# Optimization experiments

Hardware: AMD Instinct MI355X
Metric: run time of the kernel (lower is better)

## Reference

```python
import jax, jax.numpy as jnp
import numpy as np

E_DIM = 640   # RNA-FM embedding dim
H = 256       # hidden_dim
L = 3         # num_gcn_layers
LN_EPS = 1e-5


def _layer_norm(x, g, b):
    mu = jnp.mean(x, axis=-1, keepdims=True)
    var = jnp.mean((x - mu) ** 2, axis=-1, keepdims=True)
    return (x - mu) * jax.lax.rsqrt(var + LN_EPS) * g + b


def setup_inputs() -> dict:
    key = jax.random.key(0)
    ks = jax.random.split(key, 20)
    B, S = 4, 256

    def w(k, shape):
        fan_in = shape[-2] if len(shape) >= 2 else shape[-1]
        return jax.random.normal(k, shape, dtype=jnp.float32) / np.sqrt(fan_in)

    inp = {
        "embeddings": jax.random.normal(ks[0], (B, S, E_DIM), dtype=jnp.float32),
        "bp_priors": jax.random.uniform(ks[1], (B, S, S), dtype=jnp.float32),
        "sequence_lengths": jnp.full((B,), S, dtype=jnp.int32),
        # FeatureEncoder: Linear(640, 512) -> ReLU -> Linear(512, 256)
        "enc_w1": w(ks[2], (E_DIM, 2 * H)), "enc_b1": jnp.zeros((2 * H,), jnp.float32),
        "enc_w2": w(ks[3], (2 * H, H)),     "enc_b2": jnp.zeros((H,), jnp.float32),
        # GCN layers (stacked over L)
        "gcn_wself": w(ks[4], (L, H, H)), "gcn_bself": jnp.zeros((L, H), jnp.float32),
        "gcn_wedge": w(ks[5], (L, H, H)), "gcn_bedge": jnp.zeros((L, H), jnp.float32),
        "gcn_ln_g": jnp.ones((L, H), jnp.float32), "gcn_ln_b": jnp.zeros((L, H), jnp.float32),
        # PairwiseScorer MLP: Linear(2H+1, H) -> ReLU -> Linear(H, H//2) -> ReLU -> Linear(H//2, 1)
        "mlp_w1": w(ks[6], (2 * H + 1, H)), "mlp_b1": jnp.zeros((H,), jnp.float32),
        "mlp_w2": w(ks[7], (H, H // 2)),    "mlp_b2": jnp.zeros((H // 2,), jnp.float32),
        "mlp_w3": w(ks[8], (H // 2, 1)),    "mlp_b3": jnp.zeros((1,), jnp.float32),
    }
    return inp


def reference(embeddings, bp_priors, sequence_lengths,
              enc_w1, enc_b1, enc_w2, enc_b2,
              gcn_wself, gcn_bself, gcn_wedge, gcn_bedge, gcn_ln_g, gcn_ln_b,
              mlp_w1, mlp_b1, mlp_w2, mlp_b2, mlp_w3, mlp_b3):
    # FeatureEncoder
    h = jax.nn.relu(embeddings @ enc_w1 + enc_b1) @ enc_w2 + enc_b2  # [B,S,H]

    # GCN layers: self GEMM + adjacency (bp_priors) aggregated neighbor GEMM
    for l in range(L):
        self_f = h @ gcn_wself[l] + gcn_bself[l]
        neigh_f = jnp.einsum('bij,bjh->bih', bp_priors, h @ gcn_wedge[l] + gcn_bedge[l])
        h = _layer_norm(jax.nn.relu(self_f + neigh_f), gcn_ln_g[l], gcn_ln_b[l])

    # PairwiseScorer: concat([node_i, node_j, prior]) @ W1 split into three partial products
    # (mathematically identical to the expand-concat-MLP in the torch module).
    hi = h @ mlp_w1[:H]           # [B,S,H] contribution of node_i
    hj = h @ mlp_w1[H:2 * H]      # [B,S,H] contribution of node_j
    p = jax.nn.relu(hi[:, :, None, :] + hj[:, None, :, :]
                    + bp_priors[..., None] * mlp_w1[2 * H] + mlp_b1)  # [B,S,S,H]
    p = jax.nn.relu(p @ mlp_w2 + mlp_b2)                              # [B,S,S,H//2]
    bp_scores = (p @ mlp_w3 + mlp_b3)[..., 0]                         # [B,S,S]
    return bp_scores
```

## Files before the change

### kernel.cpp

```cpp
#include <hip/hip_runtime.h>

typedef __attribute__((ext_vector_type(8))) short short8;
typedef __attribute__((ext_vector_type(4))) float f32x4;

__device__ __forceinline__ unsigned short f2bf(float x) {
    union { float f; unsigned u; } v; v.f = x;
    unsigned r = v.u + 0x7FFF + ((v.u >> 16) & 1);
    return (unsigned short)(r >> 16);
}
__device__ __forceinline__ float bf2f(unsigned short h) {
    union { unsigned u; float f; } v; v.u = ((unsigned)h) << 16;
    return v.f;
}

template<bool RELU>
__global__ __launch_bounds__(256)
void gemm32(const float* __restrict__ A, const float* __restrict__ B0,
            const float* __restrict__ bias0, float* __restrict__ C0,
            const float* __restrict__ B1, const float* __restrict__ bias1,
            float* __restrict__ C1,
            int M, int N, int K, int aB, int bB, int cB, int nxHalf)
{
    int bx = blockIdx.x;
    const float* B = B0; const float* bias = bias0; float* C = C0;
    if (nxHalf && bx >= nxHalf) { bx -= nxHalf; B = B1; bias = bias1; C = C1; }
    A += (long)blockIdx.z * aB;
    B += (long)blockIdx.z * bB;
    C += (long)blockIdx.z * cB;
    const int m0 = blockIdx.y * 32, n0 = bx * 64;

    __shared__ __align__(16) float As[32][36];
    __shared__ __align__(16) float Bs[32][68];
    const int tid = threadIdx.x;
    const int tx = tid & 15, ty = tid >> 4;
    float acc[2][4] = {};

    for (int k0 = 0; k0 < K; k0 += 32) {
        {
            int row = tid >> 3, kq = (tid & 7) << 2;
            float4 v = *(const float4*)&A[(long)(m0 + row) * K + k0 + kq];
            As[kq + 0][row] = v.x; As[kq + 1][row] = v.y;
            As[kq + 2][row] = v.z; As[kq + 3][row] = v.w;
        }
#pragma unroll
        for (int q = 0; q < 2; ++q) {
            int f = tid * 2 + q;
            int kk = f >> 4, nn = (f & 15) << 2;
            *(float4*)&Bs[kk][nn] = *(const float4*)&B[(long)(k0 + kk) * N + n0 + nn];
        }
        __syncthreads();
#pragma unroll
        for (int k = 0; k < 32; ++k) {
            float2 a2 = *(const float2*)&As[k][ty * 2];
            float4 b4 = *(const float4*)&Bs[k][tx * 4];
            acc[0][0] += a2.x * b4.x; acc[0][1] += a2.x * b4.y;
            acc[0][2] += a2.x * b4.z; acc[0][3] += a2.x * b4.w;
            acc[1][0] += a2.y * b4.x; acc[1][1] += a2.y * b4.y;
            acc[1][2] += a2.y * b4.z; acc[1][3] += a2.y * b4.w;
        }
        __syncthreads();
    }

#pragma unroll
    for (int i = 0; i < 2; ++i) {
        int m = m0 + ty * 2 + i;
#pragma unroll
        for (int j = 0; j < 4; ++j) {
            int n = n0 + tx * 4 + j;
            float v = acc[i][j];
            if (bias) v += bias[n];
            if (RELU) v = fmaxf(v, 0.f);
            C[(long)m * N + n] = v;
        }
    }
}

__global__ __launch_bounds__(256)
void add_relu_ln(const float* __restrict__ a, const float* __restrict__ b,
                 const float* __restrict__ g, const float* __restrict__ bb,
                 float* __restrict__ o)
{
    const int row = blockIdx.x, t = threadIdx.x;
    const long idx = (long)row * 256 + t;
    float x = fmaxf(a[idx] + b[idx], 0.f);
    float s = x, s2 = x * x;
#pragma unroll
    for (int off = 1; off < 64; off <<= 1) {
        s  += __shfl_xor(s,  off, 64);
        s2 += __shfl_xor(s2, off, 64);
    }
    __shared__ float ws1[4], ws2[4];
    const int wid = t >> 6, lane = t & 63;
    if (lane == 0) { ws1[wid] = s; ws2[wid] = s2; }
    __syncthreads();
    s  = ws1[0] + ws1[1] + ws1[2] + ws1[3];
    s2 = ws2[0] + ws2[1] + ws2[2] + ws2[3];
    const float mu  = s * (1.f / 256.f);
    const float var = s2 * (1.f / 256.f) - mu * mu;
    o[idx] = (x - mu) * rsqrtf(var + 1e-5f) * g[t] + bb[t];
}

__global__ __launch_bounds__(256)
void split_w2t(const float* __restrict__ w2, short* __restrict__ w2th,
               short* __restrict__ w2tl)
{
    int e = blockIdx.x * 256 + threadIdx.x;
    int k = e >> 7, n = e & 127;
    float x = w2[k * 128 + n];
    unsigned short h = f2bf(x);
    unsigned short lo = f2bf(x - bf2f(h));
    w2th[n * 256 + k] = (short)h;
    w2tl[n * 256 + k] = (short)lo;
}

__global__ __launch_bounds__(256)
void pairwise_mfma(const float* __restrict__ hia, const float* __restrict__ hja,
                   const float* __restrict__ bp,
                   const float* __restrict__ c,
                   const float* __restrict__ b1,
                   const short* __restrict__ w2th, const short* __restrict__ w2tl,
                   const float* __restrict__ b2,
                   const float* __restrict__ w3,
                   const float* __restrict__ b3,
                   float* __restrict__ out)
{
    const int b = blockIdx.z, ib0 = blockIdx.y * 2, jb = blockIdx.x;
    const int tid = threadIdx.x;
    const int l = tid & 63, wid = tid >> 6;
    const int wm0 = (wid & 1) * 64, wn0 = (wid >> 1) * 64;

    __shared__ __align__(16) short Ph[128 * 32];
    __shared__ __align__(16) short Pl[128 * 32];
    __shared__ __align__(16) float hjs[64][36];
    __shared__ __align__(16) float his[2][36];
    __shared__ __align__(16) float cs[32];
    __shared__ __align__(16) float b1s[32];
    __shared__ float bpv[128];
    __shared__ float red[128][2];

    if (tid < 128) {
        int i = ib0 + (tid >> 6), j = jb * 64 + (tid & 63);
        bpv[tid] = bp[((long)(b * 256 + i)) * 256 + j];
    }

    f32x4 acc[4][4] = {};

    for (int kt = 0; kt < 8; ++kt) {
        const int k0 = kt * 32;
#pragma unroll
        for (int q = 0; q < 2; ++q) {
            int f = tid * 2 + q;
            int row = f >> 3, kq = (f & 7) << 2;
            *(float4*)&hjs[row][kq] =
                *(const float4*)&hja[((long)(b * 256 + jb * 64 + row)) * 256 + k0 + kq];
        }
        if (tid < 16) {
            int row = tid >> 3, kq = (tid & 7) << 2;
            *(float4*)&his[row][kq] =
                *(const float4*)&hia[((long)(b * 256 + ib0 + row)) * 256 + k0 + kq];
        } else if (tid < 24) {
            int f = tid - 16;
            *(float4*)&cs[f * 4] = *(const float4*)&c[k0 + f * 4];
        } else if (tid < 32) {
            int f = tid - 24;
            *(float4*)&b1s[f * 4] = *(const float4*)&b1[k0 + f * 4];
        }
        __syncthreads();

        {
            const int p = tid >> 1, kb = (tid & 1) << 4;
            const int ii = p >> 6, jj = p & 63;
            const float bw = bpv[p];
            const int swz = (p & 7) << 4;
            char* phc = (char*)Ph;
            char* plc = (char*)Pl;
#pragma unroll
            for (int q = 0; q < 4; ++q) {
                float4 hv = *(const float4*)&hjs[jj][kb + q * 4];
                float4 iv = *(const float4*)&his[ii][kb + q * 4];
                float4 cv = *(const float4*)&cs[kb + q * 4];
                float4 bv = *(const float4*)&b1s[kb + q * 4];
                float xs[4];
                xs[0] = fmaxf(iv.x + hv.x + bw * cv.x + bv.x, 0.f);
                xs[1] = fmaxf(iv.y + hv.y + bw * cv.y + bv.y, 0.f);
                xs[2] = fmaxf(iv.z + hv.z + bw * cv.z + bv.z, 0.f);
                xs[3] = fmaxf(iv.w + hv.w + bw * cv.w + bv.w, 0.f);
                unsigned hw[4], lw[4];
#pragma unroll
                for (int e = 0; e < 4; ++e) {
                    unsigned short hh = f2bf(xs[e]);
                    unsigned short ll = f2bf(xs[e] - bf2f(hh));
                    hw[e] = hh; lw[e] = ll;
                }
                int base = p * 64 + (kb + q * 4) * 2;
                *(unsigned*)(phc + ((base    ) ^ swz)) = hw[0] | (hw[1] << 16);
                *(unsigned*)(phc + ((base + 4) ^ swz)) = hw[2] | (hw[3] << 16);
                *(unsigned*)(plc + ((base    ) ^ swz)) = lw[0] | (lw[1] << 16);
                *(unsigned*)(plc + ((base + 4) ^ swz)) = lw[2] | (lw[3] << 16);
            }
        }
        __syncthreads();

        short8 ah[4], al[4], bh[4], bl[4];
        const int g = l >> 4, ln = l & 15;
#pragma unroll
        for (int mf = 0; mf < 4; ++mf) {
            int row = wm0 + mf * 16 + ln;
            int off = (row * 64 + g * 16) ^ ((row & 7) << 4);
            ah[mf] = *(const short8*)((const char*)Ph + off);
            al[mf] = *(const short8*)((const char*)Pl + off);
        }
#pragma unroll
        for (int nf = 0; nf < 4; ++nf) {
            int col = wn0 + nf * 16 + ln;
            long boff = (long)col * 256 + k0 + g * 8;
            bh[nf] = *(const short8*)(w2th + boff);
            bl[nf] = *(const short8*)(w2tl + boff);
        }
#pragma unroll
        for (int mf = 0; mf < 4; ++mf)
#pragma unroll
            for (int nf = 0; nf < 4; ++nf) {
                acc[mf][nf] = __builtin_amdgcn_mfma_f32_16x16x32_bf16(
                    ah[mf], bh[nf], acc[mf][nf], 0, 0, 0);
                acc[mf][nf] = __builtin_amdgcn_mfma_f32_16x16x32_bf16(
                    ah[mf], bl[nf], acc[mf][nf], 0, 0, 0);
                acc[mf][nf] = __builtin_amdgcn_mfma_f32_16x16x32_bf16(
                    al[mf], bh[nf], acc[mf][nf], 0, 0, 0);
            }
        __syncthreads();
    }

    const int g = l >> 4, ln = l & 15;
    float b2v[4], w3v[4];
#pragma unroll
    for (int nf = 0; nf < 4; ++nf) {
        int col = wn0 + nf * 16 + ln;
        b2v[nf] = b2[col];
        w3v[nf] = w3[col];
    }
#pragma unroll
    for (int mf = 0; mf < 4; ++mf) {
#pragma unroll
        for (int r = 0; r < 4; ++r) {
            float s = 0.f;
#pragma unroll
            for (int nf = 0; nf < 4; ++nf)
                s += fmaxf(acc[mf][nf][r] + b2v[nf], 0.f) * w3v[nf];
            s += __shfl_xor(s, 1, 64);
            s += __shfl_xor(s, 2, 64);
            s += __shfl_xor(s, 4, 64);
            s += __shfl_xor(s, 8, 64);
            if (ln == 0)
                red[wm0 + mf * 16 + g * 4 + r][wid >> 1] = s;
        }
    }
    __syncthreads();
    if (tid < 128) {
        int i = ib0 + (tid >> 6), j = jb * 64 + (tid & 63);
        out[((long)(b * 256 + i)) * 256 + j] = red[tid][0] + red[tid][1] + b3[0];
    }
}

extern "C" void kernel_launch(void* const* d_in, const int* in_sizes, int n_in,
                              void* d_out, int out_size, void* d_ws, size_t ws_size,
                              hipStream_t stream)
{
    const float* emb   = (const float*)d_in[0];
    const float* bp    = (const float*)d_in[1];
    const float* ew1   = (const float*)d_in[3];
    const float* eb1   = (const float*)d_in[4];
    const float* ew2   = (const float*)d_in[5];
    const float* eb2   = (const float*)d_in[6];
    const float* wself = (const float*)d_in[7];
    const float* bself = (const float*)d_in[8];
    const float* wedge = (const float*)d_in[9];
    const float* bedge = (const float*)d_in[10];
    const float* lng   = (const float*)d_in[11];
    const float* lnb   = (const float*)d_in[12];
    const float* mw1   = (const float*)d_in[13];
    const float* mb1   = (const float*)d_in[14];
    const float* mw2   = (const float*)d_in[15];
    const float* mb2   = (const float*)d_in[16];
    const float* mw3   = (const float*)d_in[17];
    const float* mb3   = (const float*)d_in[18];
    float* out = (float*)d_out;

    float* ws = (float*)d_ws;
    float* h1 = ws;
    float* h  = h1 + 524288;
    float* sf = h  + 262144;
    float* eg = sf + 262144;
    float* ng = eg + 262144;
    float* hi = ng + 262144;
    float* hj = hi + 262144;
    short* w2th = (short*)h1;
    short* w2tl = w2th + 32768;

    dim3 blk(256);

    gemm32<true ><<<dim3(8, 32, 1), blk, 0, stream>>>(emb, ew1, eb1, h1,
        nullptr, nullptr, nullptr, 1024, 512, 640, 0, 0, 0, 0);
    gemm32<false><<<dim3(4, 32, 1), blk, 0, stream>>>(h1, ew2, eb2, h,
        nullptr, nullptr, nullptr, 1024, 256, 512, 0, 0, 0, 0);

    split_w2t<<<dim3(128), blk, 0, stream>>>(mw2, w2th, w2tl);

    for (int lyr = 0; lyr < 3; ++lyr) {
        gemm32<false><<<dim3(8, 32, 1), blk, 0, stream>>>(h,
            wself + lyr * 65536, bself + lyr * 256, sf,
            wedge + lyr * 65536, bedge + lyr * 256, eg,
            1024, 256, 256, 0, 0, 0, 4);
        gemm32<false><<<dim3(4, 8, 4), blk, 0, stream>>>(bp, eg, nullptr, ng,
            nullptr, nullptr, nullptr, 256, 256, 256, 65536, 65536, 65536, 0);
        add_relu_ln<<<dim3(1024), blk, 0, stream>>>(sf, ng,
            lng + lyr * 256, lnb + lyr * 256, h);
    }

    gemm32<false><<<dim3(8, 32, 1), blk, 0, stream>>>(h,
        mw1, nullptr, hi, mw1 + 65536, nullptr, hj,
        1024, 256, 256, 0, 0, 0, 4);

    pairwise_mfma<<<dim3(4, 128, 4), blk, 0, stream>>>(hi, hj, bp,
        mw1 + 131072, mb1, w2th, w2tl, mb2, mw3, mb3, out);
}
```

Before: 353.7 us.

## Move dense GEMMs to split-bf16 MFMA and double-buffer pairwise kernel

```diff
diff --git a/kernel.cpp b/kernel.cpp
--- a/kernel.cpp
+++ b/kernel.cpp
@@ -12,47 +12,207 @@
     union { unsigned u; float f; } v; v.u = ((unsigned)h) << 16;
     return v.f;
 }
+__device__ __forceinline__ void gload_lds16(const void* g, void* l) {
+    __builtin_amdgcn_global_load_lds(
+        (const __attribute__((address_space(1))) unsigned*)g,
+        (__attribute__((address_space(3))) unsigned*)l, 16, 0, 0);
+}
+#define MFMA16(a, b, c) __builtin_amdgcn_mfma_f32_16x16x32_bf16((a), (b), (c), 0, 0, 0)
+
+#define OFF_EW1H 0
+#define OFF_EW1L 327680
+#define OFF_EW2H 655360
+#define OFF_EW2L 786432
+#define OFF_WSH  917504
+#define OFF_WSL  1114112
+#define OFF_WEH  1310720
+#define OFF_WEL  1507328
+#define OFF_M1IH 1703936
+#define OFF_M1IL 1769472
+#define OFF_M1JH 1835008
+#define OFF_M1JL 1900544
+#define OFF_W2H  1966080
+#define OFF_W2L  1998848
+#define SPLIT_TOTAL 2031616
+
+__global__ __launch_bounds__(256)
+void wsplit(const float* __restrict__ ew1, const float* __restrict__ ew2,
+            const float* __restrict__ wself, const float* __restrict__ wedge,
+            const float* __restrict__ mw1, const float* __restrict__ w2,
+            short* __restrict__ o)
+{
+    long e = (long)blockIdx.x * 256 + threadIdx.x;
+    float x; long dh, dl;
+    if (e < 327680) {
+        int k = e >> 9, n = e & 511;
+        x = ew1[e]; dh = OFF_EW1H + (long)n * 640 + k; dl = OFF_EW1L + (long)n * 640 + k;
+    } else if ((e -= 327680) < 131072) {
+        int k = e >> 8, n = e & 255;
+        x = ew2[e]; dh = OFF_EW2H + (long)n * 512 + k; dl = OFF_EW2L + (long)n * 512 + k;
+    } else if ((e -= 131072) < 196608) {
+        int lyr = e >> 16, r = e & 65535, k = r >> 8, n = r & 255;
+        x = wself[e]; long d = (long)lyr * 65536 + n * 256 + k;
+        dh = OFF_WSH + d; dl = OFF_WSL + d;
+    } else if ((e -= 196608) < 196608) {
+        int lyr = e >> 16, r = e & 65535, k = r >> 8, n = r & 255;
+        x = wedge[e]; long d = (long)lyr * 65536 + n * 256 + k;
+        dh = OFF_WEH + d; dl = OFF_WEL + d;
+    } else if ((e -= 196608) < 65536) {
+        int k = e >> 8, n = e & 255;
+        x = mw1[e]; dh = OFF_M1IH + (long)n * 256 + k; dl = OFF_M1IL + (long)n * 256 + k;
+    } else if ((e -= 65536) < 65536) {
+        int k = e >> 8, n = e & 255;
+        x = mw1[65536 + e]; dh = OFF_M1JH + (long)n * 256 + k; dl = OFF_M1JL + (long)n * 256 + k;
+    } else if ((e -= 65536) < 32768) {
+        int k = e >> 7, n = e & 127;
+        x = w2[e]; dh = OFF_W2H + (long)n * 256 + k; dl = OFF_W2L + (long)n * 256 + k;
+    } else return;
+    unsigned short h = f2bf(x);
+    unsigned short lo = f2bf(x - bf2f(h));
+    o[dh] = (short)h; o[dl] = (short)lo;
+}
 
 template<bool RELU>
+__global__ __launch_bounds__(256, 4)
+void gemm_mfma(const float* __restrict__ A,
+               const short* __restrict__ BTh0, const short* __restrict__ BTl0,
+               const float* __restrict__ bias0, float* __restrict__ C0,
+               const short* __restrict__ BTh1, const short* __restrict__ BTl1,
+               const float* __restrict__ bias1, float* __restrict__ C1,
+               int M, int N, int K, int nxHalf)
+{
+    int bx = blockIdx.x;
+    const short* BTh = BTh0; const short* BTl = BTl0;
+    const float* bias = bias0; float* C = C0;
+    if (nxHalf && bx >= nxHalf) { bx -= nxHalf; BTh = BTh1; BTl = BTl1; bias = bias1; C = C1; }
+    const int m0 = blockIdx.y * 64, n0 = bx * 64;
+    const int tid = threadIdx.x, l = tid & 63;
+    const int wid = tid >> 6;
+    const int wm0 = (wid & 1) * 32, wn0 = (wid >> 1) * 32;
+    const int g = l >> 4, ln = l & 15;
+
+    __shared__ __align__(16) float As[64 * 32];
+    __shared__ __align__(16) short Ah[64 * 32];
+    __shared__ __align__(16) short Al[64 * 32];
+
+    f32x4 acc[2][2] = {};
+
+    {
+        int row = tid >> 3, q = tid & 7;
+        gload_lds16(&A[(long)(m0 + row) * K + q * 4], (char*)As + tid * 16);
+        gload_lds16(&A[(long)(m0 + 32 + row) * K + q * 4], (char*)As + 4096 + tid * 16);
+    }
+    __syncthreads();
+
+    const int ktiles = K >> 5;
+    for (int kt = 0; kt < ktiles; ++kt) {
+        const int k0 = kt << 5;
+        {
+            int row = tid >> 2, kb = (tid & 3) << 3;
+            const float* src = &As[row * 32 + kb];
+            int base = row * 64 + kb * 2;
+            int swz = (row & 7) << 4;
+            char* ph = (char*)Ah; char* pl = (char*)Al;
+#pragma unroll
+            for (int q = 0; q < 2; ++q) {
+                float4 v = *(const float4*)(src + q * 4);
+                float xs[4] = {v.x, v.y, v.z, v.w};
+                unsigned hw[4], lw[4];
+#pragma unroll
+                for (int e2 = 0; e2 < 4; ++e2) {
+                    union { float f; unsigned u; } uu; uu.f = xs[e2];
+                    unsigned hbits = uu.u & 0xFFFF0000u;
+                    union { unsigned u; float f; } hh; hh.u = hbits;
+                    union { float f; unsigned u; } ll; ll.f = xs[e2] - hh.f;
+                    hw[e2] = hbits >> 16; lw[e2] = ll.u >> 16;
+                }
+                int b2 = base + q * 8;
+                *(unsigned*)(ph + ((b2    ) ^ swz)) = hw[0] | (hw[1] << 16);
+                *(unsigned*)(ph + ((b2 + 4) ^ swz)) = hw[2] | (hw[3] << 16);
+                *(unsigned*)(pl + ((b2    ) ^ swz)) = lw[0] | (lw[1] << 16);
+                *(unsigned*)(pl + ((b2 + 4) ^ swz)) = lw[2] | (lw[3] << 16);
+            }
+        }
+        __syncthreads();
+
+        short8 bh[2], bl[2], ah[2], al[2];
+#pragma unroll
+        for (int nf = 0; nf < 2; ++nf) {
+            int col = n0 + wn0 + nf * 16 + ln;
+            long bo = (long)col * K + k0 + g * 8;
+            bh[nf] = *(const short8*)(BTh + bo);
+            bl[nf] = *(const short8*)(BTl + bo);
+        }
+#pragma unroll
+        for (int mf = 0; mf < 2; ++mf) {
+            int row = wm0 + mf * 16 + ln;
+            int off = (row * 64 + g * 16) ^ ((row & 7) << 4);
+            ah[mf] = *(const short8*)((const char*)Ah + off);
+            al[mf] = *(const short8*)((const char*)Al + off);
+        }
+#pragma unroll
+        for (int mf = 0; mf < 2; ++mf)
+#pragma unroll
+            for (int nf = 0; nf < 2; ++nf) {
+                acc[mf][nf] = MFMA16(ah[mf], bh[nf], acc[mf][nf]);
+                acc[mf][nf] = MFMA16(ah[mf], bl[nf], acc[mf][nf]);
+                acc[mf][nf] = MFMA16(al[mf], bh[nf], acc[mf][nf]);
+            }
+        if (kt + 1 < ktiles) {
+            int row = tid >> 3, q = tid & 7;
+            gload_lds16(&A[(long)(m0 + row) * K + k0 + 32 + q * 4], (char*)As + tid * 16);
+            gload_lds16(&A[(long)(m0 + 32 + row) * K + k0 + 32 + q * 4], (char*)As + 4096 + tid * 16);
+        }
+        __syncthreads();
+    }
+
+#pragma unroll
+    for (int mf = 0; mf < 2; ++mf)
+#pragma unroll
+        for (int nf = 0; nf < 2; ++nf) {
+            int colb = n0 + wn0 + nf * 16 + ln;
+            float bv = bias ? bias[colb] : 0.f;
+#pragma unroll
+            for (int r = 0; r < 4; ++r) {
+                int row = m0 + wm0 + mf * 16 + g * 4 + r;
+                float v = acc[mf][nf][r] + bv;
+                if (RELU) v = fmaxf(v, 0.f);
+                C[(long)row * N + colb] = v;
+            }
+        }
+}
+
 __global__ __launch_bounds__(256)
-void gemm32(const float* __restrict__ A, const float* __restrict__ B0,
-            const float* __restrict__ bias0, float* __restrict__ C0,
-            const float* __restrict__ B1, const float* __restrict__ bias1,
-            float* __restrict__ C1,
-            int M, int N, int K, int aB, int bB, int cB, int nxHalf)
-{
-    int bx = blockIdx.x;
-    const float* B = B0; const float* bias = bias0; float* C = C0;
-    if (nxHalf && bx >= nxHalf) { bx -= nxHalf; B = B1; bias = bias1; C = C1; }
+void gemm32(const float* __restrict__ A, const float* __restrict__ B,
+            float* __restrict__ C, int M, int N, int K, int aB, int bB, int cB)
+{
     A += (long)blockIdx.z * aB;
     B += (long)blockIdx.z * bB;
     C += (long)blockIdx.z * cB;
-    const int m0 = blockIdx.y * 32, n0 = bx * 64;
-
-    __shared__ __align__(16) float As[32][36];
-    __shared__ __align__(16) float Bs[32][68];
+    const int m0 = blockIdx.y * 32, n0 = blockIdx.x * 64;
+    __shared__ __align__(16) float As2[32][36];
+    __shared__ __align__(16) float Bs2[32][68];
     const int tid = threadIdx.x;
     const int tx = tid & 15, ty = tid >> 4;
     float acc[2][4] = {};
-
     for (int k0 = 0; k0 < K; k0 += 32) {
         {
             int row = tid >> 3, kq = (tid & 7) << 2;
             float4 v = *(const float4*)&A[(long)(m0 + row) * K + k0 + kq];
-            As[kq + 0][row] = v.x; As[kq + 1][row] = v.y;
-            As[kq + 2][row] = v.z; As[kq + 3][row] = v.w;
+            As2[kq + 0][row] = v.x; As2[kq + 1][row] = v.y;
+            As2[kq + 2][row] = v.z; As2[kq + 3][row] = v.w;
         }
 #pragma unroll
         for (int q = 0; q < 2; ++q) {
             int f = tid * 2 + q;
             int kk = f >> 4, nn = (f & 15) << 2;
-            *(float4*)&Bs[kk][nn] = *(const float4*)&B[(long)(k0 + kk) * N + n0 + nn];
+            *(float4*)&Bs2[kk][nn] = *(const float4*)&B[(long)(k0 + kk) * N + n0 + nn];
         }
         __syncthreads();
 #pragma unroll
         for (int k = 0; k < 32; ++k) {
-            float2 a2 = *(const float2*)&As[k][ty * 2];
-            float4 b4 = *(const float4*)&Bs[k][tx * 4];
+            float2 a2 = *(const float2*)&As2[k][ty * 2];
+            float4 b4 = *(const float4*)&Bs2[k][tx * 4];
             acc[0][0] += a2.x * b4.x; acc[0][1] += a2.x * b4.y;
             acc[0][2] += a2.x * b4.z; acc[0][3] += a2.x * b4.w;
             acc[1][0] += a2.y * b4.x; acc[1][1] += a2.y * b4.y;
@@ -60,18 +220,12 @@
         }
         __syncthreads();
     }
-
 #pragma unroll
     for (int i = 0; i < 2; ++i) {
         int m = m0 + ty * 2 + i;
 #pragma unroll
-        for (int j = 0; j < 4; ++j) {
-            int n = n0 + tx * 4 + j;
-            float v = acc[i][j];
-            if (bias) v += bias[n];
-            if (RELU) v = fmaxf(v, 0.f);
-            C[(long)m * N + n] = v;
-        }
+        for (int j = 0; j < 4; ++j)
+            C[(long)m * N + n0 + tx * 4 + j] = acc[i][j];
     }
 }
 
@@ -100,138 +254,133 @@
     o[idx] = (x - mu) * rsqrtf(var + 1e-5f) * g[t] + bb[t];
 }
 
-__global__ __launch_bounds__(256)
-void split_w2t(const float* __restrict__ w2, short* __restrict__ w2th,
-               short* __restrict__ w2tl)
-{
-    int e = blockIdx.x * 256 + threadIdx.x;
-    int k = e >> 7, n = e & 127;
-    float x = w2[k * 128 + n];
-    unsigned short h = f2bf(x);
-    unsigned short lo = f2bf(x - bf2f(h));
-    w2th[n * 256 + k] = (short)h;
-    w2tl[n * 256 + k] = (short)lo;
-}
-
-__global__ __launch_bounds__(256)
+#define BUILD_P(KT, BUF)                                                        \
+    {                                                                           \
+        const int p = tid >> 1, kb = (tid & 1) << 4;                            \
+        const int ii = p >> 6, jj = p & 63;                                     \
+        const float bw = bpv[p];                                                \
+        const int k0b = (KT) * 32;                                              \
+        const int swz = (p & 7) << 4;                                           \
+        char* ph = (char*)&Ph[BUF][0];                                          \
+        char* pl = (char*)&Pl[BUF][0];                                          \
+        _Pragma("unroll")                                                       \
+        for (int q = 0; q < 4; ++q) {                                           \
+            float4 hv = *(const float4*)&hjs[jj * 32 + kb + q * 4];             \
+            float4 iv = *(const float4*)&his[ii][k0b + kb + q * 4];             \
+            float4 cv = *(const float4*)&cs[k0b + kb + q * 4];                  \
+            float4 bv = *(const float4*)&b1s[k0b + kb + q * 4];                 \
+            float xs[4];                                                        \
+            xs[0] = fmaxf(iv.x + hv.x + bw * cv.x + bv.x, 0.f);                 \
+            xs[1] = fmaxf(iv.y + hv.y + bw * cv.y + bv.y, 0.f);                 \
+            xs[2] = fmaxf(iv.z + hv.z + bw * cv.z + bv.z, 0.f);                 \
+            xs[3] = fmaxf(iv.w + hv.w + bw * cv.w + bv.w, 0.f);                 \
+            unsigned hw[4], lw[4];                                              \
+            _Pragma("unroll")                                                   \
+            for (int e2 = 0; e2 < 4; ++e2) {                                    \
+                union { float f; unsigned u; } uu; uu.f = xs[e2];               \
+                unsigned hbits = uu.u & 0xFFFF0000u;                            \
+                union { unsigned u; float f; } hh; hh.u = hbits;                \
+                union { float f; unsigned u; } llu; llu.f = xs[e2] - hh.f;      \
+                hw[e2] = hbits >> 16; lw[e2] = llu.u >> 16;                     \
+            }                                                                   \
+            int baseb = p * 64 + (kb + q * 4) * 2;                              \
+            *(unsigned*)(ph + ((baseb    ) ^ swz)) = hw[0] | (hw[1] << 16);     \
+            *(unsigned*)(ph + ((baseb + 4) ^ swz)) = hw[2] | (hw[3] << 16);     \
+            *(unsigned*)(pl + ((baseb    ) ^ swz)) = lw[0] | (lw[1] << 16);     \
+            *(unsigned*)(pl + ((baseb + 4) ^ swz)) = lw[2] | (lw[3] << 16);     \
+        }                                                                       \
+    }
+
+#define LOAD_B(K0)                                                              \
+    _Pragma("unroll")                                                           \
+    for (int nf = 0; nf < 4; ++nf) {                                            \
+        int col = wn0 + nf * 16 + ln;                                           \
+        long bo = (long)col * 256 + (K0) + g * 8;                               \
+        bh[nf] = *(const short8*)(w2th + bo);                                   \
+        bl[nf] = *(const short8*)(w2tl + bo);                                   \
+    }
+
+__global__ __launch_bounds__(256, 3)
 void pairwise_mfma(const float* __restrict__ hia, const float* __restrict__ hja,
                    const float* __restrict__ bp,
-                   const float* __restrict__ c,
-                   const float* __restrict__ b1,
+                   const float* __restrict__ c, const float* __restrict__ b1,
                    const short* __restrict__ w2th, const short* __restrict__ w2tl,
-                   const float* __restrict__ b2,
-                   const float* __restrict__ w3,
-                   const float* __restrict__ b3,
-                   float* __restrict__ out)
+                   const float* __restrict__ b2, const float* __restrict__ w3,
+                   const float* __restrict__ b3, float* __restrict__ out)
 {
     const int b = blockIdx.z, ib0 = blockIdx.y * 2, jb = blockIdx.x;
-    const int tid = threadIdx.x;
-    const int l = tid & 63, wid = tid >> 6;
+    const int tid = threadIdx.x, l = tid & 63, wid = tid >> 6;
     const int wm0 = (wid & 1) * 64, wn0 = (wid >> 1) * 64;
-
-    __shared__ __align__(16) short Ph[128 * 32];
-    __shared__ __align__(16) short Pl[128 * 32];
-    __shared__ __align__(16) float hjs[64][36];
-    __shared__ __align__(16) float his[2][36];
-    __shared__ __align__(16) float cs[32];
-    __shared__ __align__(16) float b1s[32];
+    const int g = l >> 4, ln = l & 15;
+
+    __shared__ __align__(16) short Ph[2][128 * 32];
+    __shared__ __align__(16) short Pl[2][128 * 32];
+    __shared__ __align__(16) float hjs[64 * 32];
+    __shared__ __align__(16) float his[2][256];
+    __shared__ __align__(16) float cs[256];
+    __shared__ __align__(16) float b1s[256];
     __shared__ float bpv[128];
     __shared__ float red[128][2];
 
     if (tid < 128) {
         int i = ib0 + (tid >> 6), j = jb * 64 + (tid & 63);
         bpv[tid] = bp[((long)(b * 256 + i)) * 256 + j];
-    }
+        int r = tid >> 6, kq = (tid & 63) << 2;
+        *(float4*)&his[r][kq] = *(const float4*)&hia[((long)(b * 256 + ib0 + r)) * 256 + kq];
+    } else if (tid < 192) {
+        int kq = (tid - 128) << 2;
+        *(float4*)&cs[kq] = *(const float4*)&c[kq];
+    } else {
+        int kq = (tid - 192) << 2;
+        *(float4*)&b1s[kq] = *(const float4*)&b1[kq];
+    }
+    {
+        int row = tid >> 3, q = tid & 7;
+        long gbase = ((long)(b * 256 + jb * 64 + row)) * 256 + q * 4;
+        gload_lds16(&hja[gbase], (char*)hjs + tid * 16);
+        gload_lds16(&hja[gbase + 32 * 256], (char*)hjs + 4096 + tid * 16);
+    }
+    __syncthreads();
+
+    short8 bh[4], bl[4];
+    LOAD_B(0);
+    BUILD_P(0, 0);
+    __syncthreads();
 
     f32x4 acc[4][4] = {};
 
     for (int kt = 0; kt < 8; ++kt) {
-        const int k0 = kt * 32;
-#pragma unroll
-        for (int q = 0; q < 2; ++q) {
-            int f = tid * 2 + q;
-            int row = f >> 3, kq = (f & 7) << 2;
-            *(float4*)&hjs[row][kq] =
-                *(const float4*)&hja[((long)(b * 256 + jb * 64 + row)) * 256 + k0 + kq];
-        }
-        if (tid < 16) {
-            int row = tid >> 3, kq = (tid & 7) << 2;
-            *(float4*)&his[row][kq] =
-                *(const float4*)&hia[((long)(b * 256 + ib0 + row)) * 256 + k0 + kq];
-        } else if (tid < 24) {
-            int f = tid - 16;
-            *(float4*)&cs[f * 4] = *(const float4*)&c[k0 + f * 4];
-        } else if (tid < 32) {
-            int f = tid - 24;
-            *(float4*)&b1s[f * 4] = *(const float4*)&b1[k0 + f * 4];
-        }
-        __syncthreads();
-
-        {
-            const int p = tid >> 1, kb = (tid & 1) << 4;
-            const int ii = p >> 6, jj = p & 63;
-            const float bw = bpv[p];
-            const int swz = (p & 7) << 4;
-            char* phc = (char*)Ph;
-            char* plc = (char*)Pl;
-#pragma unroll
-            for (int q = 0; q < 4; ++q) {
-                float4 hv = *(const float4*)&hjs[jj][kb + q * 4];
-                float4 iv = *(const float4*)&his[ii][kb + q * 4];
-                float4 cv = *(const float4*)&cs[kb + q * 4];
-                float4 bv = *(const float4*)&b1s[kb + q * 4];
-                float xs[4];
-                xs[0] = fmaxf(iv.x + hv.x + bw * cv.x + bv.x, 0.f);
-                xs[1] = fmaxf(iv.y + hv.y + bw * cv.y + bv.y, 0.f);
-                xs[2] = fmaxf(iv.z + hv.z + bw * cv.z + bv.z, 0.f);
-                xs[3] = fmaxf(iv.w + hv.w + bw * cv.w + bv.w, 0.f);
-                unsigned hw[4], lw[4];
-#pragma unroll
-                for (int e = 0; e < 4; ++e) {
-                    unsigned short hh = f2bf(xs[e]);
-                    unsigned short ll = f2bf(xs[e] - bf2f(hh));
-                    hw[e] = hh; lw[e] = ll;
-                }
-                int base = p * 64 + (kb + q * 4) * 2;
-                *(unsigned*)(phc + ((base    ) ^ swz)) = hw[0] | (hw[1] << 16);
-                *(unsigned*)(phc + ((base + 4) ^ swz)) = hw[2] | (hw[3] << 16);
-                *(unsigned*)(plc + ((base    ) ^ swz)) = lw[0] | (lw[1] << 16);
-                *(unsigned*)(plc + ((base + 4) ^ swz)) = lw[2] | (lw[3] << 16);
-            }
-        }
-        __syncthreads();
-
-        short8 ah[4], al[4], bh[4], bl[4];
-        const int g = l >> 4, ln = l & 15;
+        const int cur = kt & 1;
+        if (kt < 7) {
+            int row = tid >> 3, q = tid & 7;
+            long gbase = ((long)(b * 256 + jb * 64 + row)) * 256 + (kt + 1) * 32 + q * 4;
+            gload_lds16(&hja[gbase], (char*)hjs + tid * 16);
+            gload_lds16(&hja[gbase + 32 * 256], (char*)hjs + 4096 + tid * 16);
+        }
+        short8 ah[4], al[4];
 #pragma unroll
         for (int mf = 0; mf < 4; ++mf) {
             int row = wm0 + mf * 16 + ln;
             int off = (row * 64 + g * 16) ^ ((row & 7) << 4);
-            ah[mf] = *(const short8*)((const char*)Ph + off);
-            al[mf] = *(const short8*)((const char*)Pl + off);
-        }
-#pragma unroll
-        for (int nf = 0; nf < 4; ++nf) {
-            int col = wn0 + nf * 16 + ln;
-            long boff = (long)col * 256 + k0 + g * 8;
-            bh[nf] = *(const short8*)(w2th + boff);
-            bl[nf] = *(const short8*)(w2tl + boff);
+            ah[mf] = *(const short8*)((const char*)&Ph[cur][0] + off);
+            al[mf] = *(const short8*)((const char*)&Pl[cur][0] + off);
         }
 #pragma unroll
         for (int mf = 0; mf < 4; ++mf)
 #pragma unroll
             for (int nf = 0; nf < 4; ++nf) {
-                acc[mf][nf] = __builtin_amdgcn_mfma_f32_16x16x32_bf16(
-                    ah[mf], bh[nf], acc[mf][nf], 0, 0, 0);
-                acc[mf][nf] = __builtin_amdgcn_mfma_f32_16x16x32_bf16(
-                    ah[mf], bl[nf], acc[mf][nf], 0, 0, 0);
-                acc[mf][nf] = __builtin_amdgcn_mfma_f32_16x16x32_bf16(
-                    al[mf], bh[nf], acc[mf][nf], 0, 0, 0);
+                acc[mf][nf] = MFMA16(ah[mf], bh[nf], acc[mf][nf]);
+                acc[mf][nf] = MFMA16(ah[mf], bl[nf], acc[mf][nf]);
+                acc[mf][nf] = MFMA16(al[mf], bh[nf], acc[mf][nf]);
             }
         __syncthreads();
-    }
-
-    const int g = l >> 4, ln = l & 15;
+        if (kt < 7) {
+            LOAD_B((kt + 1) * 32);
+            BUILD_P(kt + 1, cur ^ 1);
+        }
+        __syncthreads();
+    }
+
     float b2v[4], w3v[4];
 #pragma unroll
     for (int nf = 0; nf < 4; ++nf) {
@@ -294,33 +443,35 @@
     float* ng = eg + 262144;
     float* hi = ng + 262144;
     float* hj = hi + 262144;
-    short* w2th = (short*)h1;
-    short* w2tl = w2th + 32768;
+    short* sb = (short*)(hj + 262144);
 
     dim3 blk(256);
 
-    gemm32<true ><<<dim3(8, 32, 1), blk, 0, stream>>>(emb, ew1, eb1, h1,
-        nullptr, nullptr, nullptr, 1024, 512, 640, 0, 0, 0, 0);
-    gemm32<false><<<dim3(4, 32, 1), blk, 0, stream>>>(h1, ew2, eb2, h,
-        nullptr, nullptr, nullptr, 1024, 256, 512, 0, 0, 0, 0);
-
-    split_w2t<<<dim3(128), blk, 0, stream>>>(mw2, w2th, w2tl);
+    wsplit<<<dim3(3968), blk, 0, stream>>>(ew1, ew2, wself, wedge, mw1, mw2, sb);
+
+    gemm_mfma<true ><<<dim3(8, 16), blk, 0, stream>>>(emb,
+        sb + OFF_EW1H, sb + OFF_EW1L, eb1, h1,
+        nullptr, nullptr, nullptr, nullptr, 1024, 512, 640, 0);
+    gemm_mfma<false><<<dim3(4, 16), blk, 0, stream>>>(h1,
+        sb + OFF_EW2H, sb + OFF_EW2L, eb2, h,
+        nullptr, nullptr, nullptr, nullptr, 1024, 256, 512, 0);
 
     for (int lyr = 0; lyr < 3; ++lyr) {
-        gemm32<false><<<dim3(8, 32, 1), blk, 0, stream>>>(h,
-            wself + lyr * 65536, bself + lyr * 256, sf,
-            wedge + lyr * 65536, bedge + lyr * 256, eg,
-            1024, 256, 256, 0, 0, 0, 4);
-        gemm32<false><<<dim3(4, 8, 4), blk, 0, stream>>>(bp, eg, nullptr, ng,
-            nullptr, nullptr, nullptr, 256, 256, 256, 65536, 65536, 65536, 0);
+        gemm_mfma<false><<<dim3(8, 16), blk, 0, stream>>>(h,
+            sb + OFF_WSH + lyr * 65536, sb + OFF_WSL + lyr * 65536, bself + lyr * 256, sf,
+            sb + OFF_WEH + lyr * 65536, sb + OFF_WEL + lyr * 65536, bedge + lyr * 256, eg,
+            1024, 256, 256, 4);
+        gemm32<<<dim3(4, 8, 4), blk, 0, stream>>>(bp, eg, ng, 256, 256, 256,
+                                                  65536, 65536, 65536);
         add_relu_ln<<<dim3(1024), blk, 0, stream>>>(sf, ng,
             lng + lyr * 256, lnb + lyr * 256, h);
     }
 
-    gemm32<false><<<dim3(8, 32, 1), blk, 0, stream>>>(h,
-        mw1, nullptr, hi, mw1 + 65536, nullptr, hj,
-        1024, 256, 256, 0, 0, 0, 4);
+    gemm_mfma<false><<<dim3(8, 16), blk, 0, stream>>>(h,
+        sb + OFF_M1IH, sb + OFF_M1IL, nullptr, hi,
+        sb + OFF_M1JH, sb + OFF_M1JL, nullptr, hj,
+        1024, 256, 256, 4);
 
     pairwise_mfma<<<dim3(4, 128, 4), blk, 0, stream>>>(hi, hj, bp,
-        mw1 + 131072, mb1, w2th, w2tl, mb2, mw3, mb3, out);
-}
+        mw1 + 131072, mb1, sb + OFF_W2H, sb + OFF_W2L, mb2, mw3, mb3, out);
+}
```

Result: no change. 356.8 us (+0.9%).
